# Kernel optimization log

Hardware: AMD Instinct MI355X
Metric: run time of the kernel (lower is better)

## Reference

```python
import jax, jax.numpy as jnp
import numpy as np

NUM_USERS = 100000
NUM_MOVIES = 50000
NUM_EDGES = 4000000
USER_FEAT = 24
MOVIE_FEAT = 404
HID = 64
GENRES = 3


def setup_inputs() -> dict:
    key = jax.random.key(0)
    ks = jax.random.split(key, 16)
    inp = {
        'x_user': jax.random.normal(ks[0], (NUM_USERS, USER_FEAT), jnp.float32),
        'x_movie': jax.random.normal(ks[1], (NUM_MOVIES, MOVIE_FEAT), jnp.float32),
        'edge_src': jax.random.randint(ks[2], (NUM_EDGES,), 0, NUM_USERS, jnp.int32),
        'edge_dst': jax.random.randint(ks[3], (NUM_EDGES,), 0, NUM_MOVIES, jnp.int32),
        'W_user': jax.random.normal(ks[4], (HID, USER_FEAT), jnp.float32) * 0.1,
        'b_user': jax.random.normal(ks[5], (HID,), jnp.float32) * 0.1,
        'W_movie': jax.random.normal(ks[6], (HID, MOVIE_FEAT), jnp.float32) * 0.05,
        'b_movie': jax.random.normal(ks[7], (HID,), jnp.float32) * 0.1,
        'Wl1_um': jax.random.normal(ks[8], (HID, HID), jnp.float32) * 0.1,
        'bl1_um': jax.random.normal(ks[9], (HID,), jnp.float32) * 0.1,
        'Wr1_um': jax.random.normal(ks[10], (HID, HID), jnp.float32) * 0.1,
        'Wl1_mu': jax.random.normal(ks[11], (HID, HID), jnp.float32) * 0.1,
        'bl1_mu': jax.random.normal(ks[12], (HID,), jnp.float32) * 0.1,
        'Wr1_mu': jax.random.normal(ks[13], (HID, HID), jnp.float32) * 0.1,
        'Wl2_um': jax.random.normal(ks[14], (GENRES, HID), jnp.float32) * 0.1,
        'bl2_um': jnp.zeros((GENRES,), jnp.float32),
        'Wr2_um': jax.random.normal(ks[15], (GENRES, HID), jnp.float32) * 0.1,
    }
    return inp


def _mean_agg(src_x, src_idx, dst_idx, num_dst):
    # gather messages [E, C], scatter-sum to dst, divide by degree (mean aggr)
    msg = src_x[src_idx]
    s = jax.ops.segment_sum(msg, dst_idx, num_segments=num_dst)
    cnt = jax.ops.segment_sum(jnp.ones_like(dst_idx, jnp.float32), dst_idx, num_segments=num_dst)
    return s / jnp.maximum(cnt, 1.0)[:, None]


def _sage(agg, x_dst, Wl, bl, Wr):
    # SAGEConv: lin_l(mean_aggr(x_j)) + lin_r(x_dst); bias only on lin_l
    return agg @ Wl.T + bl + x_dst @ Wr.T


def reference(x_user, x_movie, edge_src, edge_dst, W_user, b_user, W_movie, b_movie,
              Wl1_um, bl1_um, Wr1_um, Wl1_mu, bl1_mu, Wr1_mu, Wl2_um, bl2_um, Wr2_um):
    nu, nm = x_user.shape[0], x_movie.shape[0]
    # input projections
    hu = x_user @ W_user.T + b_user    # [U, H]
    hm = x_movie @ W_movie.T + b_movie  # [M, H]
    # layer 1 (hetero: one SAGEConv per edge type; undirected -> both directions)
    m1 = _sage(_mean_agg(hu, edge_src, edge_dst, nm), hm, Wl1_um, bl1_um, Wr1_um)
    u1 = _sage(_mean_agg(hm, edge_dst, edge_src, nu), hu, Wl1_mu, bl1_mu, Wr1_mu)
    m1 = jax.nn.relu(m1)
    u1 = jax.nn.relu(u1)
    # dropout is identity in eval mode
    # layer 2: only movie output is returned
    out = _sage(_mean_agg(u1, edge_src, edge_dst, nm), m1, Wl2_um, bl2_um, Wr2_um)
    return out
```

## Files before the change

kernel.cpp:

```cpp
#include <hip/hip_runtime.h>


constexpr int NU = 100000;
constexpr int NM = 50000;
constexpr int NE = 4000000;
constexpr int FU = 24;
constexpr int FM = 404;
constexpr int HD = 64;

constexpr int BSH = 8;
constexpr int MBK = (NM + 255) >> BSH;
constexpr int UBK = (NU + 255) >> BSH;
constexpr int NBK = MBK + UBK;
constexpr int EPB = 8192;
constexpr int CAPE = 28672;

static inline size_t alignup(size_t x) { return (x + 255) & ~size_t(255); }

__device__ __forceinline__ float bf2f(unsigned short h) {
  return __uint_as_float(((unsigned int)h) << 16);
}
__device__ __forceinline__ unsigned short f2bf(float f) {
  unsigned int u = __float_as_uint(f);
  u = (u + 0x7FFFu + ((u >> 16) & 1u)) >> 16;
  return (unsigned short)u;
}
__device__ __forceinline__ float2 unpk(unsigned u) {
  return make_float2(__uint_as_float(u << 16), __uint_as_float(u & 0xFFFF0000u));
}
__device__ __forceinline__ float fp8dec(unsigned v) {
  unsigned u = ((v & 0x80u) << 24) | ((v & 0x7Fu) << 20);
  return __uint_as_float(u) * 0x1p120f;
}
__device__ __forceinline__ unsigned char f2fp8(float f) {
  float a = fminf(fabsf(f), 448.0f);
  unsigned u = __float_as_uint(a * 0x1p-120f);
  u = u + 0x7FFFFu + ((u >> 20) & 1u);
  return (unsigned char)(((u >> 20) & 0x7Fu) | ((__float_as_uint(f) >> 24) & 0x80u));
}

typedef __attribute__((ext_vector_type(2))) float f2v;

#if __has_builtin(__builtin_amdgcn_cvt_pk_f32_fp8)
#define FP8_HW 1
#endif

__device__ __forceinline__ f2v fp8lo(unsigned w) {
#ifdef FP8_HW
  return __builtin_amdgcn_cvt_pk_f32_fp8(w, false);
#else
  f2v r; r.x = fp8dec(w); r.y = fp8dec(w >> 8); return r;
#endif
}
__device__ __forceinline__ f2v fp8hi(unsigned w) {
#ifdef FP8_HW
  return __builtin_amdgcn_cvt_pk_f32_fp8(w, true);
#else
  f2v r; r.x = fp8dec(w >> 16); r.y = fp8dec(w >> 24); return r;
#endif
}
__device__ __forceinline__ unsigned pk2bf(f2v v) {
  return (unsigned)f2bf(v.x) | ((unsigned)f2bf(v.y) << 16);
}

using bf16x8 = __attribute__((ext_vector_type(8))) short;
using f32x4  = __attribute__((ext_vector_type(4))) float;


__global__ __launch_bounds__(256) void histB_kernel(const int* __restrict__ src,
                                                    const int* __restrict__ dst,
                                                    int* __restrict__ bh) {
  __shared__ int h[NBK];
  for (int i = threadIdx.x; i < NBK; i += 256) h[i] = 0;
  __syncthreads();
  int idx = blockIdx.x * 256 + threadIdx.x;
  int stride = gridDim.x * 256;
  for (int i = idx; i < NE; i += stride) {
    atomicAdd(&h[dst[i] >> BSH], 1);
    atomicAdd(&h[MBK + (src[i] >> BSH)], 1);
  }
  __syncthreads();
  for (int i = threadIdx.x; i < NBK; i += 256) {
    int c = h[i];
    if (c) atomicAdd(&bh[i], c);
  }
}

__global__ __launch_bounds__(1024) void scanB_kernel(const int* __restrict__ bh,
                                                     int* __restrict__ bbase_m,
                                                     int* __restrict__ bbase_u,
                                                     int* __restrict__ bcur_m,
                                                     int* __restrict__ bcur_u) {
  __shared__ int tmp[1024];
  int t = threadIdx.x;
  int vm = (t < MBK) ? bh[t] : 0;
  tmp[t] = vm;
  __syncthreads();
  for (int off = 1; off < 1024; off <<= 1) {
    int v = (t >= off) ? tmp[t - off] : 0;
    __syncthreads();
    tmp[t] += v;
    __syncthreads();
  }
  if (t < MBK) {
    int e = tmp[t] - vm;
    bbase_m[t] = e; bcur_m[t] = e;
    if (t == MBK - 1) bbase_m[MBK] = tmp[t];
  }
  __syncthreads();
  int vu = (t < UBK) ? bh[MBK + t] : 0;
  tmp[t] = vu;
  __syncthreads();
  for (int off = 1; off < 1024; off <<= 1) {
    int v = (t >= off) ? tmp[t - off] : 0;
    __syncthreads();
    tmp[t] += v;
    __syncthreads();
  }
  if (t < UBK) {
    int e = tmp[t] - vu;
    bbase_u[t] = e; bcur_u[t] = e;
    if (t == UBK - 1) bbase_u[UBK] = tmp[t];
  }
}

__global__ __launch_bounds__(1024) void passA_kernel(
    const int* __restrict__ src, const int* __restrict__ dst,
    int* __restrict__ bcur_m, int* __restrict__ bcur_u,
    unsigned* __restrict__ stage_m, unsigned* __restrict__ stage_u) {
  __shared__ int hB[NBK];
  __shared__ int cntB[NBK];
  __shared__ int gB[NBK];
  __shared__ int tmp[1024];
  __shared__ unsigned binM[EPB];
  __shared__ unsigned binU[EPB];
  int t = threadIdx.x;
  for (int i = t; i < NBK; i += 1024) hB[i] = 0;
  __syncthreads();
  int e0 = blockIdx.x * EPB + t;
  int sv[8], dv[8], rm[8], ru[8];
#pragma unroll
  for (int k = 0; k < 8; ++k) {
    int e = e0 + k * 1024;
    if (e < NE) {
      int s = src[e], d = dst[e];
      sv[k] = s; dv[k] = d;
      rm[k] = atomicAdd(&hB[d >> BSH], 1);
      ru[k] = atomicAdd(&hB[MBK + (s >> BSH)], 1);
    } else {
      sv[k] = -1;
    }
  }
  __syncthreads();
  int cm = (t < MBK) ? hB[t] : 0;
  tmp[t] = cm;
  __syncthreads();
  for (int off = 1; off < 1024; off <<= 1) {
    int v = (t >= off) ? tmp[t - off] : 0;
    __syncthreads();
    tmp[t] += v;
    __syncthreads();
  }
  int lofsM = tmp[t] - cm;
  __syncthreads();
  int cu_ = (t < UBK) ? hB[MBK + t] : 0;
  tmp[t] = cu_;
  __syncthreads();
  for (int off = 1; off < 1024; off <<= 1) {
    int v = (t >= off) ? tmp[t - off] : 0;
    __syncthreads();
    tmp[t] += v;
    __syncthreads();
  }
  int lofsU = tmp[t] - cu_;
  __syncthreads();
  if (t < MBK) { cntB[t] = cm; hB[t] = lofsM; }
  if (t < UBK) { cntB[MBK + t] = cu_; hB[MBK + t] = lofsU; }
  __syncthreads();
#pragma unroll
  for (int k = 0; k < 8; ++k) {
    if (sv[k] >= 0) {
      int s = sv[k], d = dv[k];
      binM[hB[d >> BSH] + rm[k]] = ((unsigned)(d & 255) << 24) | (unsigned)s;
      binU[hB[MBK + (s >> BSH)] + ru[k]] = ((unsigned)(s & 255) << 24) | (unsigned)d;
    }
  }
  __syncthreads();
  for (int b = t; b < NBK; b += 1024) {
    int cc = cntB[b];
    if (cc) {
      int gb = (b < MBK) ? atomicAdd(&bcur_m[b], cc) : atomicAdd(&bcur_u[b - MBK], cc);
      gB[b] = gb - hB[b];
    }
  }
  __syncthreads();
  int wv = t >> 6, ln = t & 63;
  for (int b = wv; b < MBK; b += 16) {
    int cc = cntB[b], lo = hB[b], go = hB[b] + gB[b];
    for (int j = ln; j < cc; j += 64) stage_m[go + j] = binM[lo + j];
  }
  for (int b = wv; b < UBK; b += 16) {
    int cc = cntB[MBK + b], lo = hB[MBK + b], go = hB[MBK + b] + gB[MBK + b];
    for (int j = ln; j < cc; j += 64) stage_u[go + j] = binU[lo + j];
  }
}

__global__ __launch_bounds__(1024) void passB_kernel(
    const int* __restrict__ bbase_m, const int* __restrict__ bbase_u,
    const unsigned* __restrict__ stage_m, const unsigned* __restrict__ stage_u,
    int* __restrict__ csr_m, int* __restrict__ csr_u,
    int* __restrict__ rp_m, int* __restrict__ rp_u) {
  __shared__ int cnt[256];
  __shared__ int sc[256];
  extern __shared__ unsigned sbuf[];
  int b = blockIdx.x;
  const unsigned* stage; int* csr; int* rp; int idbase, ntot, bb, be;
  if (b < MBK) {
    stage = stage_m; csr = csr_m; rp = rp_m;
    idbase = b << BSH; ntot = NM;
    bb = bbase_m[b]; be = bbase_m[b + 1];
  } else {
    int c = b - MBK;
    stage = stage_u; csr = csr_u; rp = rp_u;
    idbase = c << BSH; ntot = NU;
    bb = bbase_u[c]; be = bbase_u[c + 1];
  }
  int nloc = min(256, ntot - idbase);
  int t = threadIdx.x;
  int span = be - bb;
  if (t < 256) cnt[t] = 0;
  __syncthreads();
  for (int j = bb + t; j < be; j += 1024) atomicAdd(&cnt[stage[j] >> 24], 1);
  __syncthreads();
  int c0 = (t < 256) ? cnt[t] : 0;
  if (t < 256) sc[t] = c0;
  __syncthreads();
  for (int off = 1; off < 256; off <<= 1) {
    int v = 0;
    if (t < 256 && t >= off) v = sc[t - off];
    __syncthreads();
    if (t < 256) sc[t] += v;
    __syncthreads();
  }
  if (t < nloc) {
    rp[idbase + t] = bb + sc[t] - c0;
    cnt[t] = sc[t] - c0;
  }
  if (t == 0 && idbase + nloc == ntot) rp[ntot] = be;
  __syncthreads();
  if (span <= CAPE) {
    for (int j = bb + t; j < be; j += 1024) {
      unsigned e = stage[j];
      int pos = atomicAdd(&cnt[e >> 24], 1);
      sbuf[pos] = e & 0xFFFFFFu;
    }
    __syncthreads();
    for (int j = t; j < span; j += 1024) csr[bb + j] = (int)sbuf[j];
  } else {
    for (int j = bb + t; j < be; j += 1024) {
      unsigned e = stage[j];
      int pos = atomicAdd(&cnt[e >> 24], 1);
      csr[bb + pos] = (int)(e & 0xFFFFFFu);
    }
  }
}


__global__ void convXu_kernel(const float* __restrict__ xu, unsigned char* __restrict__ xu8) {
  int i = blockIdx.x * 256 + threadIdx.x;
  if (i < NU * 32) {
    int r = i >> 5, c = i & 31;
    xu8[i] = (c < FU) ? f2fp8(xu[r * FU + c]) : 0;
  }
}

__global__ void convXu16_kernel(const float* __restrict__ xu, unsigned short* __restrict__ xb) {
  int i = blockIdx.x * 256 + threadIdx.x;
  if (i < NU * 32) {
    int r = i >> 5, c = i & 31;
    unsigned short v = 0;
    if (c < FU) v = f2bf(xu[r * FU + c]);
    else if (c == 31) v = 0x3F80;
    xb[i] = v;
  }
}

__global__ void convW_kernel(const float* __restrict__ W, unsigned short* __restrict__ Wb,
                             int n) {
  int i = blockIdx.x * 256 + threadIdx.x;
  if (i < n) Wb[i] = f2bf(W[i]);
}

__global__ void convWum_kernel(const float* __restrict__ Wl, const float* __restrict__ Wu,
                               const float* __restrict__ bu, const float* __restrict__ Wr,
                               unsigned short* __restrict__ W96) {
  int i = blockIdx.x * 256 + threadIdx.x;
  if (i >= 64 * 96) return;
  int h = i / 96, k = i - h * 96;
  float v = 0.f;
  if (k < FU) {
    for (int j = 0; j < 64; ++j) v += Wl[h * 64 + j] * Wu[j * FU + k];
  } else if (k == 31) {
    for (int j = 0; j < 64; ++j) v += Wl[h * 64 + j] * bu[j];
  } else if (k >= 32) {
    v = Wr[h * 64 + (k - 32)];
  }
  W96[i] = f2bf(v);
}

__global__ void convWmu_kernel(const float* __restrict__ Wl, const float* __restrict__ Wr,
                               const float* __restrict__ Wu, const float* __restrict__ bu,
                               unsigned short* __restrict__ W96) {
  int i = blockIdx.x * 256 + threadIdx.x;
  if (i >= 64 * 96) return;
  int h = i / 96, k = i - h * 96;
  float v = 0.f;
  if (k < 64) {
    v = Wl[h * 64 + k];
  } else if (k < 64 + FU) {
    for (int j = 0; j < 64; ++j) v += Wr[h * 64 + j] * Wu[j * FU + (k - 64)];
  } else if (k == 95) {
    for (int j = 0; j < 64; ++j) v += Wr[h * 64 + j] * bu[j];
  }
  W96[i] = f2bf(v);
}

__global__ __launch_bounds__(256) void proj_movie_kernel(
    const float* __restrict__ xm, const unsigned short* __restrict__ Wb,
    const float* __restrict__ bm, unsigned short* __restrict__ hm,
    unsigned char* __restrict__ hm8) {
  __shared__ unsigned short Xs[64][72];
  __shared__ unsigned short Ws[64][72];
  int t = threadIdx.x;
  int lane = t & 63, wid = t >> 6;
  int row0 = blockIdx.x * 64;
  int r0 = wid * 16;
  f32x4 acc[4];
#pragma unroll
  for (int nt = 0; nt < 4; ++nt) acc[nt] = (f32x4){0.f, 0.f, 0.f, 0.f};

  for (int k0 = 0; k0 < 448; k0 += 64) {
    int kc = min(64, FM - k0);
    __syncthreads();
    for (int i = t; i < 1024; i += 256) {
      int r = i >> 4, c4 = i & 15;
      float4 v = make_float4(0.f, 0.f, 0.f, 0.f);
      if (c4 * 4 < kc && row0 + r < NM)
        v = *(const float4*)(xm + (size_t)(row0 + r) * FM + k0 + c4 * 4);
      ushort4 o;
      o.x = f2bf(v.x); o.y = f2bf(v.y); o.z = f2bf(v.z); o.w = f2bf(v.w);
      *(ushort4*)&Xs[r][c4 * 4] = o;
    }
    for (int i = t; i < 1024; i += 256) {
      int h = i >> 4, c4 = i & 15;
      uint2 v = make_uint2(0u, 0u);
      if (c4 * 4 < kc)
        v = *(const uint2*)(Wb + (size_t)h * FM + k0 + c4 * 4);
      *(uint2*)&Ws[h][c4 * 4] = v;
    }
    __syncthreads();
#pragma unroll
    for (int kk = 0; kk < 64; kk += 32) {
      bf16x8 a = *(const bf16x8*)&Xs[r0 + (lane & 15)][kk + (lane >> 4) * 8];
#pragma unroll
      for (int nt = 0; nt < 4; ++nt) {
        bf16x8 b = *(const bf16x8*)&Ws[nt * 16 + (lane & 15)][kk + (lane >> 4) * 8];
        acc[nt] = __builtin_amdgcn_mfma_f32_16x16x32_bf16(a, b, acc[nt], 0, 0, 0);
      }
    }
  }
  int col = lane & 15;
  int rbase = r0 + (lane >> 4) * 4;
#pragma unroll
  for (int nt = 0; nt < 4; ++nt) {
    float b = bm[nt * 16 + col];
#pragma unroll
    for (int j = 0; j < 4; ++j) {
      int row = row0 + rbase + j;
      if (row < NM) {
        float v = acc[nt][j] + b;
        hm[(size_t)row * HD + nt * 16 + col] = f2bf(v);
        hm8[(size_t)row * HD + nt * 16 + col] = f2fp8(v);
      }
    }
  }
}


__global__ __launch_bounds__(256) void agg24_kernel(
    const unsigned char* __restrict__ xu8, const int* __restrict__ rp,
    const int* __restrict__ csr, unsigned short* __restrict__ a24, int n) {
  int wid = threadIdx.x >> 6, lane = threadIdx.x & 63;
  int row = blockIdx.x * 4 + wid;
  if (row >= n) return;
  int beg = rp[row], end = rp[row + 1];
  int g = lane >> 2;
  int fq = lane & 3;
  f2v a01 = {0.f, 0.f}, a23 = {0.f, 0.f}, a45 = {0.f, 0.f}, a67 = {0.f, 0.f};
  int i = beg;
  for (; i + 32 <= end; i += 32) {
    int n0 = csr[i + g];
    int n1 = csr[i + 16 + g];
    uint2 w0 = *(const uint2*)(xu8 + (size_t)n0 * 32 + fq * 8);
    uint2 w1 = *(const uint2*)(xu8 + (size_t)n1 * 32 + fq * 8);
    a01 += fp8lo(w0.x) + fp8lo(w1.x);
    a23 += fp8hi(w0.x) + fp8hi(w1.x);
    a45 += fp8lo(w0.y) + fp8lo(w1.y);
    a67 += fp8hi(w0.y) + fp8hi(w1.y);
  }
  for (; i < end; i += 16) {
    int idx = i + g;
    if (idx < end) {
      uint2 w = *(const uint2*)(xu8 + (size_t)csr[idx] * 32 + fq * 8);
      a01 += fp8lo(w.x); a23 += fp8hi(w.x);
      a45 += fp8lo(w.y); a67 += fp8hi(w.y);
    }
  }
  float a[8] = {a01.x, a01.y, a23.x, a23.y, a45.x, a45.y, a67.x, a67.y};
#pragma unroll
  for (int off = 4; off < 64; off <<= 1)
#pragma unroll
    for (int j = 0; j < 8; ++j) a[j] += __shfl_xor(a[j], off);
  if (g == 0) {
    float inv = 1.0f / fmaxf((float)(end - beg), 1.0f);
    uint4 o;
    o.x = (unsigned)f2bf(a[0] * inv) | ((unsigned)f2bf(a[1] * inv) << 16);
    o.y = (unsigned)f2bf(a[2] * inv) | ((unsigned)f2bf(a[3] * inv) << 16);
    o.z = (unsigned)f2bf(a[4] * inv) | ((unsigned)f2bf(a[5] * inv) << 16);
    o.w = (unsigned)f2bf(a[6] * inv) | ((unsigned)f2bf(a[7] * inv) << 16);
    if (fq == 3)
      o.w = (o.w & 0xFFFFu) | ((end > beg ? 0x3F80u : 0u) << 16);
    *(uint4*)(a24 + (size_t)row * 32 + fq * 8) = o;
  }
}


__global__ __launch_bounds__(256) void aggU_kernel(
    const unsigned char* __restrict__ tab8, const int* __restrict__ rp,
    const int* __restrict__ csr, unsigned short* __restrict__ out, int n) {
  int wid = threadIdx.x >> 6, lane = threadIdx.x & 63;
  int row = blockIdx.x * 4 + wid;
  if (row >= n) return;
  int beg = rp[row], end = rp[row + 1];
  int g = lane >> 3;
  int fq = lane & 7;
  f2v a01 = {0.f, 0.f}, a23 = {0.f, 0.f}, a45 = {0.f, 0.f}, a67 = {0.f, 0.f};
  int i = beg;
  for (; i + 16 <= end; i += 16) {
    int n0 = csr[i + g];
    int n1 = csr[i + 8 + g];
    uint2 w0 = *(const uint2*)(tab8 + (size_t)n0 * HD + fq * 8);
    uint2 w1 = *(const uint2*)(tab8 + (size_t)n1 * HD + fq * 8);
    a01 += fp8lo(w0.x) + fp8lo(w1.x);
    a23 += fp8hi(w0.x) + fp8hi(w1.x);
    a45 += fp8lo(w0.y) + fp8lo(w1.y);
    a67 += fp8hi(w0.y) + fp8hi(w1.y);
  }
  for (; i < end; i += 8) {
    int idx = i + g;
    if (idx < end) {
      uint2 w = *(const uint2*)(tab8 + (size_t)csr[idx] * HD + fq * 8);
      a01 += fp8lo(w.x); a23 += fp8hi(w.x);
      a45 += fp8lo(w.y); a67 += fp8hi(w.y);
    }
  }
  float a[8] = {a01.x, a01.y, a23.x, a23.y, a45.x, a45.y, a67.x, a67.y};
#pragma unroll
  for (int off = 8; off < 64; off <<= 1)
#pragma unroll
    for (int j = 0; j < 8; ++j) a[j] += __shfl_xor(a[j], off);
  if (g == 0) {
    float inv = 1.0f / fmaxf((float)(end - beg), 1.0f);
    uint4 o;
    o.x = (unsigned)f2bf(a[0] * inv) | ((unsigned)f2bf(a[1] * inv) << 16);
    o.y = (unsigned)f2bf(a[2] * inv) | ((unsigned)f2bf(a[3] * inv) << 16);
    o.z = (unsigned)f2bf(a[4] * inv) | ((unsigned)f2bf(a[5] * inv) << 16);
    o.w = (unsigned)f2bf(a[6] * inv) | ((unsigned)f2bf(a[7] * inv) << 16);
    *(uint4*)(out + (size_t)row * HD + fq * 8) = o;
  }
}


__global__ __launch_bounds__(256) void sage_um_kernel(
    const unsigned short* __restrict__ a24, const unsigned short* __restrict__ hm,
    const unsigned short* __restrict__ W96, const float* __restrict__ bl,
    unsigned short* __restrict__ m1, int n) {
  __shared__ unsigned short Xs[64][104];
  __shared__ unsigned short Ws[64][104];
  int t = threadIdx.x;
  int lane = t & 63, wid = t >> 6;
  int row0 = blockIdx.x * 64;
  int r0 = wid * 16;
  for (int i = t; i < 768; i += 256) {
    int h = i / 12, g = i - h * 12;
    *(uint4*)&Ws[h][g * 8] = *(const uint4*)(W96 + (size_t)h * 96 + g * 8);
  }
  for (int i = t; i < 768; i += 256) {
    int r = i / 12, g = i - r * 12;
    uint4 v = make_uint4(0u, 0u, 0u, 0u);
    if (row0 + r < n) {
      if (g < 4) v = *(const uint4*)(a24 + (size_t)(row0 + r) * 32 + g * 8);
      else       v = *(const uint4*)(hm + (size_t)(row0 + r) * HD + (g - 4) * 8);
    }
    *(uint4*)&Xs[r][g * 8] = v;
  }
  __syncthreads();
  f32x4 acc[4];
#pragma unroll
  for (int nt = 0; nt < 4; ++nt) acc[nt] = (f32x4){0.f, 0.f, 0.f, 0.f};
#pragma unroll
  for (int kk = 0; kk < 96; kk += 32) {
    bf16x8 a = *(const bf16x8*)&Xs[r0 + (lane & 15)][kk + (lane >> 4) * 8];
#pragma unroll
    for (int nt = 0; nt < 4; ++nt) {
      bf16x8 b = *(const bf16x8*)&Ws[nt * 16 + (lane & 15)][kk + (lane >> 4) * 8];
      acc[nt] = __builtin_amdgcn_mfma_f32_16x16x32_bf16(a, b, acc[nt], 0, 0, 0);
    }
  }
  int col = lane & 15;
  int rbase = r0 + (lane >> 4) * 4;
#pragma unroll
  for (int nt = 0; nt < 4; ++nt) {
    float b = bl[nt * 16 + col];
#pragma unroll
    for (int j = 0; j < 4; ++j) {
      int row = row0 + rbase + j;
      if (row < n)
        m1[(size_t)row * HD + nt * 16 + col] = f2bf(fmaxf(acc[nt][j] + b, 0.f));
    }
  }
}


__global__ __launch_bounds__(256) void sage96u_kernel(
    const unsigned short* __restrict__ agg, const unsigned short* __restrict__ xb,
    const unsigned short* __restrict__ W96, const float* __restrict__ bl,
    unsigned short* __restrict__ u1, int n) {
  __shared__ unsigned short Xs[64][104];
  __shared__ unsigned short Ws[64][104];
  int t = threadIdx.x;
  int lane = t & 63, wid = t >> 6;
  int row0 = blockIdx.x * 64;
  int r0 = wid * 16;
  for (int i = t; i < 768; i += 256) {
    int h = i / 12, g = i - h * 12;
    *(uint4*)&Ws[h][g * 8] = *(const uint4*)(W96 + (size_t)h * 96 + g * 8);
  }
  for (int i = t; i < 768; i += 256) {
    int r = i / 12, g = i - r * 12;
    uint4 v = make_uint4(0u, 0u, 0u, 0u);
    if (row0 + r < n) {
      if (g < 8) v = *(const uint4*)(agg + (size_t)(row0 + r) * HD + g * 8);
      else       v = *(const uint4*)(xb + (size_t)(row0 + r) * 32 + (g - 8) * 8);
    }
    *(uint4*)&Xs[r][g * 8] = v;
  }
  __syncthreads();
  f32x4 acc[4];
#pragma unroll
  for (int nt = 0; nt < 4; ++nt) acc[nt] = (f32x4){0.f, 0.f, 0.f, 0.f};
#pragma unroll
  for (int kk = 0; kk < 96; kk += 32) {
    bf16x8 a = *(const bf16x8*)&Xs[r0 + (lane & 15)][kk + (lane >> 4) * 8];
#pragma unroll
    for (int nt = 0; nt < 4; ++nt) {
      bf16x8 b = *(const bf16x8*)&Ws[nt * 16 + (lane & 15)][kk + (lane >> 4) * 8];
      acc[nt] = __builtin_amdgcn_mfma_f32_16x16x32_bf16(a, b, acc[nt], 0, 0, 0);
    }
  }
  int col = lane & 15;
  int rbase = r0 + (lane >> 4) * 4;
#pragma unroll
  for (int nt = 0; nt < 4; ++nt) {
    float b = bl[nt * 16 + col];
#pragma unroll
    for (int j = 0; j < 4; ++j) {
      int row = row0 + rbase + j;
      if (row < n)
        u1[(size_t)row * HD + nt * 16 + col] = f2bf(fmaxf(acc[nt][j] + b, 0.f));
    }
  }
}


__global__ __launch_bounds__(256) void zproj_kernel(
    const unsigned short* __restrict__ u1, const float* __restrict__ Wl2,
    float4* __restrict__ z) {
  __shared__ float W[3][64];
  int t = threadIdx.x;
  if (t < 192) W[t / 64][t & 63] = Wl2[t];
  __syncthreads();
  int wid = t >> 6, lane = t & 63;
  int g = lane >> 4, fq = lane & 15;
  int row = blockIdx.x * 16 + wid * 4 + g;
  if (row >= NU) return;
  uint2 v = *(const uint2*)(u1 + (size_t)row * HD + fq * 4);
  float2 p0 = unpk(v.x), p1 = unpk(v.y);
  int f = fq * 4;
  float z0 = p0.x * W[0][f] + p0.y * W[0][f + 1] + p1.x * W[0][f + 2] + p1.y * W[0][f + 3];
  float z1 = p0.x * W[1][f] + p0.y * W[1][f + 1] + p1.x * W[1][f + 2] + p1.y * W[1][f + 3];
  float z2 = p0.x * W[2][f] + p0.y * W[2][f + 1] + p1.x * W[2][f + 2] + p1.y * W[2][f + 3];
#pragma unroll
  for (int off = 1; off < 16; off <<= 1) {
    z0 += __shfl_xor(z0, off);
    z1 += __shfl_xor(z1, off);
    z2 += __shfl_xor(z2, off);
  }
  if (fq == 0) z[row] = make_float4(z0, z1, z2, 0.f);
}

__global__ __launch_bounds__(256) void agg4_kernel(
    const float4* __restrict__ z, const int* __restrict__ rp,
    const int* __restrict__ csr, float4* __restrict__ zagg, int n) {
  int wid = threadIdx.x >> 6, lane = threadIdx.x & 63;
  int row = blockIdx.x * 4 + wid;
  if (row >= n) return;
  int beg = rp[row], end = rp[row + 1];
  float s0 = 0.f, s1 = 0.f, s2 = 0.f;
  for (int i = beg + lane; i < end; i += 64) {
    float4 v = z[csr[i]];
    s0 += v.x; s1 += v.y; s2 += v.z;
  }
#pragma unroll
  for (int off = 1; off < 64; off <<= 1) {
    s0 += __shfl_xor(s0, off);
    s1 += __shfl_xor(s1, off);
    s2 += __shfl_xor(s2, off);
  }
  if (lane == 0) {
    float inv = 1.0f / fmaxf((float)(end - beg), 1.0f);
    zagg[row] = make_float4(s0 * inv, s1 * inv, s2 * inv, 0.f);
  }
}

__global__ void out2_kernel(const float4* __restrict__ zagg,
                            const unsigned short* __restrict__ m1,
                            const float* __restrict__ Wr2, const float* __restrict__ bl2,
                            float* __restrict__ out, int n) {
  int wid = threadIdx.x >> 6, lane = threadIdx.x & 63;
  int row = blockIdx.x * 4 + wid;
  if (row >= n) return;
  float mm = bf2f(m1[(size_t)row * HD + lane]);
  float4 za = zagg[row];
  float zc[3] = {za.x, za.y, za.z};
#pragma unroll
  for (int g = 0; g < 3; ++g) {
    float p = mm * Wr2[g * HD + lane];
#pragma unroll
    for (int off = 32; off > 0; off >>= 1) p += __shfl_down(p, off);
    if (lane == 0) out[row * 3 + g] = p + zc[g] + bl2[g];
  }
}


extern "C" void kernel_launch(void* const* d_in, const int* in_sizes, int n_in,
                              void* d_out, int out_size, void* d_ws, size_t ws_size,
                              hipStream_t stream) {
  const float* x_user  = (const float*)d_in[0];
  const float* x_movie = (const float*)d_in[1];
  const int*   e_src   = (const int*)d_in[2];
  const int*   e_dst   = (const int*)d_in[3];
  const float* W_user  = (const float*)d_in[4];
  const float* b_user  = (const float*)d_in[5];
  const float* W_movie = (const float*)d_in[6];
  const float* b_movie = (const float*)d_in[7];
  const float* Wl1_um  = (const float*)d_in[8];
  const float* bl1_um  = (const float*)d_in[9];
  const float* Wr1_um  = (const float*)d_in[10];
  const float* Wl1_mu  = (const float*)d_in[11];
  const float* bl1_mu  = (const float*)d_in[12];
  const float* Wr1_mu  = (const float*)d_in[13];
  const float* Wl2_um  = (const float*)d_in[14];
  const float* bl2_um  = (const float*)d_in[15];
  const float* Wr2_um  = (const float*)d_in[16];
  float* outp = (float*)d_out;

  char* p = (char*)d_ws;
  size_t off = 0;
  auto take = [&](size_t bytes) { void* r = p + off; off += alignup(bytes); return r; };

  int* rp_m    = (int*)take(size_t(NM + 1) * 4);
  int* rp_u    = (int*)take(size_t(NU + 1) * 4);
  int* bh      = (int*)take(size_t(NBK) * 4);
  int* bbase_m = (int*)take(size_t(MBK + 1) * 4);
  int* bbase_u = (int*)take(size_t(UBK + 1) * 4);
  int* bcur_m  = (int*)take(size_t(MBK) * 4);
  int* bcur_u  = (int*)take(size_t(UBK) * 4);
  int* csr_m   = (int*)take(size_t(NE) * 4);
  int* csr_u   = (int*)take(size_t(NE) * 4);

  size_t ov_base = off;
  unsigned* stage_m = (unsigned*)take(size_t(NE) * 4);
  unsigned* stage_u = (unsigned*)take(size_t(NE) * 4);
  size_t stage_end = off;
  off = ov_base;
  unsigned short* hm    = (unsigned short*)take(size_t(NM) * HD * 2);
  unsigned short* u1    = (unsigned short*)take(size_t(NU) * HD * 2);
  unsigned short* m1    = (unsigned short*)take(size_t(NM) * HD * 2);
  unsigned short* aggb  = (unsigned short*)take(size_t(NU) * HD * 2);
  unsigned char*  xu8   = (unsigned char*)take(size_t(NU) * 32);
  unsigned char*  hm8   = (unsigned char*)take(size_t(NM) * HD);
  unsigned short* a24   = (unsigned short*)take(size_t(NM) * 32 * 2);
  unsigned short* xub16 = (unsigned short*)take(size_t(NU) * 32 * 2);
  if (off < stage_end) off = stage_end;
  float4* z    = (float4*)take(size_t(NU) * 16);
  float4* zagg = (float4*)take(size_t(NM) * 16);
  unsigned short* Wb    = (unsigned short*)take(size_t(HD) * FM * 2);
  unsigned short* Wum96 = (unsigned short*)take(size_t(HD) * 96 * 2);
  unsigned short* Wmu96 = (unsigned short*)take(size_t(HD) * 96 * 2);
  if (off > ws_size) return;

  const int TB = 256;

  hipMemsetAsync(bh, 0, size_t(NBK) * 4, stream);
  histB_kernel<<<512, 256, 0, stream>>>(e_src, e_dst, bh);
  scanB_kernel<<<1, 1024, 0, stream>>>(bh, bbase_m, bbase_u, bcur_m, bcur_u);
  passA_kernel<<<(NE + EPB - 1) / EPB, 1024, 0, stream>>>(e_src, e_dst, bcur_m, bcur_u,
                                                          stage_m, stage_u);
  passB_kernel<<<NBK, 1024, CAPE * 4, stream>>>(bbase_m, bbase_u, stage_m, stage_u,
                                                csr_m, csr_u, rp_m, rp_u);

  convW_kernel<<<(HD * FM + 255) / 256, 256, 0, stream>>>(W_movie, Wb, HD * FM);
  convWum_kernel<<<(64 * 96 + 255) / 256, 256, 0, stream>>>(Wl1_um, W_user, b_user,
                                                            Wr1_um, Wum96);
  convWmu_kernel<<<(64 * 96 + 255) / 256, 256, 0, stream>>>(Wl1_mu, Wr1_mu, W_user,
                                                            b_user, Wmu96);
  convXu_kernel<<<(NU * 32 + 255) / 256, 256, 0, stream>>>(x_user, xu8);
  convXu16_kernel<<<(NU * 32 + 255) / 256, 256, 0, stream>>>(x_user, xub16);
  proj_movie_kernel<<<(NM + 63) / 64, TB, 0, stream>>>(x_movie, Wb, b_movie, hm, hm8);

  agg24_kernel<<<(NM + 3) / 4, TB, 0, stream>>>(xu8, rp_m, csr_m, a24, NM);
  sage_um_kernel<<<(NM + 63) / 64, TB, 0, stream>>>(a24, hm, Wum96, bl1_um, m1, NM);

  aggU_kernel<<<(NU + 3) / 4, TB, 0, stream>>>(hm8, rp_u, csr_u, aggb, NU);
  sage96u_kernel<<<(NU + 63) / 64, TB, 0, stream>>>(aggb, xub16, Wmu96, bl1_mu, u1, NU);

  zproj_kernel<<<(NU + 15) / 16, TB, 0, stream>>>(u1, Wl2_um, z);
  agg4_kernel<<<(NM + 3) / 4, TB, 0, stream>>>(z, rp_m, csr_m, zagg, NM);
  out2_kernel<<<(NM + 3) / 4, TB, 0, stream>>>(zagg, m1, Wr2_um, bl2_um, outp, NM);
}
```

Before: 296.4 us.

## Fuse layer-2 z aggregation into movie-side layer-1 gather and unroll aggU

Moves the user-side layer-1 path and zproj ahead of the movie-side aggregation. The 24-wide fp8 user gather now also accumulates the projected z values per neighbor in the same pass over csr_m, so the separate agg4 kernel and its second walk over the 4M-edge CSR are gone. The aggU gather loop also gets a 4-way unrolled main loop for more memory parallelism. The cost is an extra scattered 4-byte z load per neighbor inside the agg24 kernel, plus more register pressure.

Result: faster. 288.8 us (-2.6%).

```diff
diff --git a/kernel.cpp b/kernel.cpp
--- a/kernel.cpp
+++ b/kernel.cpp
@@ -58,9 +58,6 @@
 #else
   f2v r; r.x = fp8dec(w >> 16); r.y = fp8dec(w >> 24); return r;
 #endif
-}
-__device__ __forceinline__ unsigned pk2bf(f2v v) {
-  return (unsigned)f2bf(v.x) | ((unsigned)f2bf(v.y) << 16);
 }
 
 using bf16x8 = __attribute__((ext_vector_type(8))) short;
@@ -387,9 +384,10 @@
 }
 
 
-__global__ __launch_bounds__(256) void agg24_kernel(
-    const unsigned char* __restrict__ xu8, const int* __restrict__ rp,
-    const int* __restrict__ csr, unsigned short* __restrict__ a24, int n) {
+__global__ __launch_bounds__(256) void agg24z_kernel(
+    const unsigned char* __restrict__ xu8, const float* __restrict__ z,
+    const int* __restrict__ rp, const int* __restrict__ csr,
+    unsigned short* __restrict__ a24, float* __restrict__ zagg, int n) {
   int wid = threadIdx.x >> 6, lane = threadIdx.x & 63;
   int row = blockIdx.x * 4 + wid;
   if (row >= n) return;
@@ -397,12 +395,14 @@
   int g = lane >> 2;
   int fq = lane & 3;
   f2v a01 = {0.f, 0.f}, a23 = {0.f, 0.f}, a45 = {0.f, 0.f}, a67 = {0.f, 0.f};
+  float az = 0.f;
   int i = beg;
   for (; i + 32 <= end; i += 32) {
     int n0 = csr[i + g];
     int n1 = csr[i + 16 + g];
     uint2 w0 = *(const uint2*)(xu8 + (size_t)n0 * 32 + fq * 8);
     uint2 w1 = *(const uint2*)(xu8 + (size_t)n1 * 32 + fq * 8);
+    az += z[n0 * 4 + fq] + z[n1 * 4 + fq];
     a01 += fp8lo(w0.x) + fp8lo(w1.x);
     a23 += fp8hi(w0.x) + fp8hi(w1.x);
     a45 += fp8lo(w0.y) + fp8lo(w1.y);
@@ -411,16 +411,20 @@
   for (; i < end; i += 16) {
     int idx = i + g;
     if (idx < end) {
-      uint2 w = *(const uint2*)(xu8 + (size_t)csr[idx] * 32 + fq * 8);
+      int nb = csr[idx];
+      uint2 w = *(const uint2*)(xu8 + (size_t)nb * 32 + fq * 8);
+      az += z[nb * 4 + fq];
       a01 += fp8lo(w.x); a23 += fp8hi(w.x);
       a45 += fp8lo(w.y); a67 += fp8hi(w.y);
     }
   }
   float a[8] = {a01.x, a01.y, a23.x, a23.y, a45.x, a45.y, a67.x, a67.y};
 #pragma unroll
-  for (int off = 4; off < 64; off <<= 1)
+  for (int off = 4; off < 64; off <<= 1) {
 #pragma unroll
     for (int j = 0; j < 8; ++j) a[j] += __shfl_xor(a[j], off);
+    az += __shfl_xor(az, off);
+  }
   if (g == 0) {
     float inv = 1.0f / fmaxf((float)(end - beg), 1.0f);
     uint4 o;
@@ -431,6 +435,7 @@
     if (fq == 3)
       o.w = (o.w & 0xFFFFu) | ((end > beg ? 0x3F80u : 0u) << 16);
     *(uint4*)(a24 + (size_t)row * 32 + fq * 8) = o;
+    zagg[row * 4 + fq] = az * inv;
   }
 }
 
@@ -446,6 +451,20 @@
   int fq = lane & 7;
   f2v a01 = {0.f, 0.f}, a23 = {0.f, 0.f}, a45 = {0.f, 0.f}, a67 = {0.f, 0.f};
   int i = beg;
+  for (; i + 32 <= end; i += 32) {
+    int n0 = csr[i + g];
+    int n1 = csr[i + 8 + g];
+    int n2 = csr[i + 16 + g];
+    int n3 = csr[i + 24 + g];
+    uint2 w0 = *(const uint2*)(tab8 + (size_t)n0 * HD + fq * 8);
+    uint2 w1 = *(const uint2*)(tab8 + (size_t)n1 * HD + fq * 8);
+    uint2 w2 = *(const uint2*)(tab8 + (size_t)n2 * HD + fq * 8);
+    uint2 w3 = *(const uint2*)(tab8 + (size_t)n3 * HD + fq * 8);
+    a01 += (fp8lo(w0.x) + fp8lo(w1.x)) + (fp8lo(w2.x) + fp8lo(w3.x));
+    a23 += (fp8hi(w0.x) + fp8hi(w1.x)) + (fp8hi(w2.x) + fp8hi(w3.x));
+    a45 += (fp8lo(w0.y) + fp8lo(w1.y)) + (fp8lo(w2.y) + fp8lo(w3.y));
+    a67 += (fp8hi(w0.y) + fp8hi(w1.y)) + (fp8hi(w2.y) + fp8hi(w3.y));
+  }
   for (; i + 16 <= end; i += 16) {
     int n0 = csr[i + g];
     int n1 = csr[i + 8 + g];
@@ -609,31 +628,7 @@
   if (fq == 0) z[row] = make_float4(z0, z1, z2, 0.f);
 }
 
-__global__ __launch_bounds__(256) void agg4_kernel(
-    const float4* __restrict__ z, const int* __restrict__ rp,
-    const int* __restrict__ csr, float4* __restrict__ zagg, int n) {
-  int wid = threadIdx.x >> 6, lane = threadIdx.x & 63;
-  int row = blockIdx.x * 4 + wid;
-  if (row >= n) return;
-  int beg = rp[row], end = rp[row + 1];
-  float s0 = 0.f, s1 = 0.f, s2 = 0.f;
-  for (int i = beg + lane; i < end; i += 64) {
-    float4 v = z[csr[i]];
-    s0 += v.x; s1 += v.y; s2 += v.z;
-  }
-#pragma unroll
-  for (int off = 1; off < 64; off <<= 1) {
-    s0 += __shfl_xor(s0, off);
-    s1 += __shfl_xor(s1, off);
-    s2 += __shfl_xor(s2, off);
-  }
-  if (lane == 0) {
-    float inv = 1.0f / fmaxf((float)(end - beg), 1.0f);
-    zagg[row] = make_float4(s0 * inv, s1 * inv, s2 * inv, 0.f);
-  }
-}
-
-__global__ void out2_kernel(const float4* __restrict__ zagg,
+__global__ void out2_kernel(const float* __restrict__ zagg,
                             const unsigned short* __restrict__ m1,
                             const float* __restrict__ Wr2, const float* __restrict__ bl2,
                             float* __restrict__ out, int n) {
@@ -641,14 +636,12 @@
   int row = blockIdx.x * 4 + wid;
   if (row >= n) return;
   float mm = bf2f(m1[(size_t)row * HD + lane]);
-  float4 za = zagg[row];
-  float zc[3] = {za.x, za.y, za.z};
 #pragma unroll
   for (int g = 0; g < 3; ++g) {
     float p = mm * Wr2[g * HD + lane];
 #pragma unroll
     for (int off = 32; off > 0; off >>= 1) p += __shfl_down(p, off);
-    if (lane == 0) out[row * 3 + g] = p + zc[g] + bl2[g];
+    if (lane == 0) out[row * 3 + g] = p + zagg[row * 4 + g] + bl2[g];
   }
 }
 
@@ -703,8 +696,8 @@
   unsigned short* a24   = (unsigned short*)take(size_t(NM) * 32 * 2);
   unsigned short* xub16 = (unsigned short*)take(size_t(NU) * 32 * 2);
   if (off < stage_end) off = stage_end;
-  float4* z    = (float4*)take(size_t(NU) * 16);
-  float4* zagg = (float4*)take(size_t(NM) * 16);
+  float* z    = (float*)take(size_t(NU) * 16);
+  float* zagg = (float*)take(size_t(NM) * 16);
   unsigned short* Wb    = (unsigned short*)take(size_t(HD) * FM * 2);
   unsigned short* Wum96 = (unsigned short*)take(size_t(HD) * 96 * 2);
   unsigned short* Wmu96 = (unsigned short*)take(size_t(HD) * 96 * 2);
@@ -729,13 +722,12 @@
   convXu16_kernel<<<(NU * 32 + 255) / 256, 256, 0, stream>>>(x_user, xub16);
   proj_movie_kernel<<<(NM + 63) / 64, TB, 0, stream>>>(x_movie, Wb, b_movie, hm, hm8);
 
-  agg24_kernel<<<(NM + 3) / 4, TB, 0, stream>>>(xu8, rp_m, csr_m, a24, NM);
-  sage_um_kernel<<<(NM + 63) / 64, TB, 0, stream>>>(a24, hm, Wum96, bl1_um, m1, NM);
-
   aggU_kernel<<<(NU + 3) / 4, TB, 0, stream>>>(hm8, rp_u, csr_u, aggb, NU);
   sage96u_kernel<<<(NU + 63) / 64, TB, 0, stream>>>(aggb, xub16, Wmu96, bl1_mu, u1, NU);
-
-  zproj_kernel<<<(NU + 15) / 16, TB, 0, stream>>>(u1, Wl2_um, z);
-  agg4_kernel<<<(NM + 3) / 4, TB, 0, stream>>>(z, rp_m, csr_m, zagg, NM);
+  zproj_kernel<<<(NU + 15) / 16, TB, 0, stream>>>(u1, Wl2_um, (float4*)z);
+
+  agg24z_kernel<<<(NM + 3) / 4, TB, 0, stream>>>(xu8, z, rp_m, csr_m, a24, zagg, NM);
+  sage_um_kernel<<<(NM + 63) / 64, TB, 0, stream>>>(a24, hm, Wum96, bl1_um, m1, NM);
+
   out2_kernel<<<(NM + 3) / 4, TB, 0, stream>>>(zagg, m1, Wr2_um, bl2_um, outp, NM);
 }
```
